# Kernel optimization log

Hardware: AMD Instinct MI355X
Metric: run time of the kernel (lower is better)

The kernel has to match this reference:

```python
import jax, jax.numpy as jnp
import numpy as np

N_PARENTS = 8
CHILDREN_PER_PARENT = 7
N_CHILDREN = N_PARENTS * CHILDREN_PER_PARENT  # 56 leaf classes
TOTAL_NODES = N_PARENTS + N_CHILDREN          # 64
BATCH = 262144


def _build_state_space():
    """Faithful port of generate_state_space for levels==2.

    Row 0 is the all-zero root state; then for each parent, one parent-only
    row, followed by one (parent, child) row per child. Shape [65, 64].
    """
    S = np.zeros((TOTAL_NODES + 1, TOTAL_NODES), dtype=np.float32)
    recorded = np.zeros(TOTAL_NODES)
    ii = 1
    for c in range(N_CHILDREN):
        p = N_CHILDREN + c // CHILDREN_PER_PARENT  # parent ids 56..63
        if recorded[p] == 0:
            S[ii, p] = 1.0
            recorded[p] = 1
            ii += 1
        S[ii, p] = 1.0
        S[ii, c] = 1.0
        ii += 1
    assert ii == TOTAL_NODES + 1, 'Invalid State Space'
    return jnp.asarray(S)


def setup_inputs() -> dict:
    key = jax.random.key(0)
    k1, k2 = jax.random.split(key)
    pred_label = jax.random.normal(k1, (BATCH, TOTAL_NODES), dtype=jnp.float32)
    gt_label = jax.random.randint(k2, (BATCH,), 0, N_CHILDREN, dtype=jnp.int32)
    return {
        'pred_label': pred_label,
        'gt_label': gt_label,
        'state_space': _build_state_space(),
    }


def reference(pred_label, gt_label, state_space):
    # index[s, b] = <state_space row s, pred_label[b]>  -> [S+1, B]
    index = state_space @ pred_label.T
    joint = jnp.exp(index)                      # [S+1, B]
    z = jnp.sum(joint, axis=0)                  # [B] partition function
    # Vectorized replacement of the per-sample Python loop:
    # rows of the state space that contain the ground-truth node.
    mask = state_space[:, gt_label] > 0         # [S+1, B]
    marginal = jnp.sum(jnp.where(mask, joint, jnp.zeros((), joint.dtype)), axis=0)  # [B]
    loss = -jnp.log(marginal / z)               # [B]
    return jnp.mean(loss)
```

## Files before the change

### kernel.cpp

```cpp
#include <hip/hip_runtime.h>


#define RPB     256
#define THREADS 256

__device__ __forceinline__ float elem(const float4& v, int j) {
    return j == 0 ? v.x : j == 1 ? v.y : j == 2 ? v.z : v.w;
}

__global__ void __launch_bounds__(THREADS) tree_loss_partial(
    const float* __restrict__ pred,
    const int*   __restrict__ gt,
    float*       __restrict__ partial,
    int rows)
{
    __shared__ float wsum[THREADS / 64];

    const int t   = threadIdx.x;
    const int row = blockIdx.x * RPB + t;

    float loss = 0.0f;
    if (row < rows) {
        const float4* p4 = (const float4*)(pred + (size_t)row * 64);

        float4 v[16];
        #pragma unroll
        for (int i = 0; i < 16; ++i) v[i] = p4[i];

        float S[8];
        #pragma unroll
        for (int p = 0; p < 8; ++p) S[p] = 0.0f;
        #pragma unroll
        for (int i = 0; i < 14; ++i) {
            #pragma unroll
            for (int j = 0; j < 4; ++j) {
                constexpr int dummy = 0; (void)dummy;
                const int col = 4 * i + j;
                S[col / 7] += __expf(elem(v[i], j));
            }
        }
        float z = 1.0f;
        #pragma unroll
        for (int p = 0; p < 8; ++p) {
            const int i = (56 + p) >> 2, j = (56 + p) & 3;
            z += __expf(elem(v[i], j)) * (1.0f + S[p]);
        }

        int g = gt[row];
        float xg = pred[(size_t)row * 64 + g];
        float xp = pred[(size_t)row * 64 + 56 + g / 7];
        loss = __logf(z) - xg - xp;
    }

    #pragma unroll
    for (int off = 32; off; off >>= 1) loss += __shfl_xor(loss, off);
    if ((t & 63) == 0) wsum[t >> 6] = loss;
    __syncthreads();
    if (t == 0) {
        float b = 0.0f;
        #pragma unroll
        for (int w = 0; w < THREADS / 64; ++w) b += wsum[w];
        partial[blockIdx.x] = b;
    }
}

__global__ void __launch_bounds__(256) tree_loss_final(
    const float* __restrict__ partial, int n,
    float* __restrict__ out, float inv)
{
    float s = 0.0f;
    for (int i = threadIdx.x; i < n; i += 256) s += partial[i];
    #pragma unroll
    for (int off = 32; off; off >>= 1) s += __shfl_xor(s, off);
    __shared__ float w[4];
    const int lane = threadIdx.x & 63;
    const int wv   = threadIdx.x >> 6;
    if (lane == 0) w[wv] = s;
    __syncthreads();
    if (threadIdx.x == 0) out[0] = (w[0] + w[1] + w[2] + w[3]) * inv;
}

extern "C" void kernel_launch(void* const* d_in, const int* in_sizes, int n_in,
                              void* d_out, int out_size, void* d_ws, size_t ws_size,
                              hipStream_t stream) {
    const float* pred = (const float*)d_in[0];
    const int*   gt   = (const int*)d_in[1];
    float* out     = (float*)d_out;
    float* partial = (float*)d_ws;
    const int rows = in_sizes[1];

    const int blocks = (rows + RPB - 1) / RPB;
    tree_loss_partial<<<blocks, THREADS, 0, stream>>>(pred, gt, partial, rows);
    tree_loss_final<<<1, 256, 0, stream>>>(partial, blocks, out, 1.0f / (float)rows);
}
```

Before: 24.56 us.

## Coalesce row loads via wave-cooperative LDS staging with two lanes per row

Each wave now cooperatively loads 32 contiguous rows with fully coalesced float4 loads, writes exp values into padded shared memory, and then has two lanes per row compute half of the partition sum each, combined with a shuffle. This replaces per-thread strided 256-byte row reads, which coalesce poorly, plus the separate scattered gathers of the ground-truth logits. The cost is LDS traffic, a doubled block count with half the rows per block, and the log of the marginal now being computed from exponentials, which can lose precision.

```diff
diff --git a/kernel.cpp b/kernel.cpp
--- a/kernel.cpp
+++ b/kernel.cpp
@@ -1,12 +1,10 @@
 #include <hip/hip_runtime.h>
 
 
-#define RPB     256
 #define THREADS 256
-
-__device__ __forceinline__ float elem(const float4& v, int j) {
-    return j == 0 ? v.x : j == 1 ? v.y : j == 2 ? v.z : v.w;
-}
+#define WROWS   32
+#define RPB     (4 * WROWS)
+#define STRIDE  65
 
 __global__ void __launch_bounds__(THREADS) tree_loss_partial(
     const float* __restrict__ pred,
@@ -14,54 +12,62 @@
     float*       __restrict__ partial,
     int rows)
 {
-    __shared__ float wsum[THREADS / 64];
+    __shared__ float lds[4 * WROWS * STRIDE];
+    __shared__ float wsum[4];
 
-    const int t   = threadIdx.x;
-    const int row = blockIdx.x * RPB + t;
+    const int t = threadIdx.x;
+    const int w = t >> 6;
+    const int l = t & 63;
+    const int waveRowBase = blockIdx.x * RPB + w * WROWS;
+    float* e_base = &lds[w * WROWS * STRIDE];
 
-    float loss = 0.0f;
-    if (row < rows) {
-        const float4* p4 = (const float4*)(pred + (size_t)row * 64);
+    const float4* p4 = (const float4*)pred + (size_t)waveRowBase * 16;
+    const bool full = (waveRowBase + WROWS <= rows);
+    float4 v[8];
+    #pragma unroll
+    for (int i = 0; i < 8; ++i) {
+        const int f = i * 64 + l;
+        v[i] = (full || waveRowBase + (f >> 4) < rows)
+                 ? p4[f] : make_float4(0.f, 0.f, 0.f, 0.f);
+    }
+    #pragma unroll
+    for (int i = 0; i < 8; ++i) {
+        const int f   = i * 64 + l;
+        const int row = f >> 4;
+        const int c4  = (f & 15) << 2;
+        float* dst = e_base + row * STRIDE + c4;
+        dst[0] = __expf(v[i].x); dst[1] = __expf(v[i].y);
+        dst[2] = __expf(v[i].z); dst[3] = __expf(v[i].w);
+    }
 
-        float4 v[16];
+    const int r  = l & 31;
+    const int hi = l >> 5;
+    const float* e  = e_base + r * STRIDE;
+    const float* ec = e + hi * 28;
+    const float* ep = e + 56 + hi * 4;
+    float zh = 0.f;
+    #pragma unroll
+    for (int p = 0; p < 4; ++p) {
+        float s = 1.f;
         #pragma unroll
-        for (int i = 0; i < 16; ++i) v[i] = p4[i];
+        for (int c = 0; c < 7; ++c) s += ec[p * 7 + c];
+        zh += ep[p] * s;
+    }
+    const float zo = __shfl_xor(zh, 32);
 
-        float S[8];
-        #pragma unroll
-        for (int p = 0; p < 8; ++p) S[p] = 0.0f;
-        #pragma unroll
-        for (int i = 0; i < 14; ++i) {
-            #pragma unroll
-            for (int j = 0; j < 4; ++j) {
-                constexpr int dummy = 0; (void)dummy;
-                const int col = 4 * i + j;
-                S[col / 7] += __expf(elem(v[i], j));
-            }
-        }
-        float z = 1.0f;
-        #pragma unroll
-        for (int p = 0; p < 8; ++p) {
-            const int i = (56 + p) >> 2, j = (56 + p) & 3;
-            z += __expf(elem(v[i], j)) * (1.0f + S[p]);
-        }
-
-        int g = gt[row];
-        float xg = pred[(size_t)row * 64 + g];
-        float xp = pred[(size_t)row * 64 + 56 + g / 7];
-        loss = __logf(z) - xg - xp;
-    }
+    const int rowg = waveRowBase + r;
+    const bool valid = (rowg < rows);
+    const int g = valid ? gt[rowg] : 0;
+    const float z = 1.f + zh + zo;
+    const float m = e[g] * e[56 + g / 7];
+    float loss = __logf(z / m);
+    loss = (hi == 0 && valid) ? loss : 0.f;
 
     #pragma unroll
     for (int off = 32; off; off >>= 1) loss += __shfl_xor(loss, off);
-    if ((t & 63) == 0) wsum[t >> 6] = loss;
+    if (l == 0) wsum[w] = loss;
     __syncthreads();
-    if (t == 0) {
-        float b = 0.0f;
-        #pragma unroll
-        for (int w = 0; w < THREADS / 64; ++w) b += wsum[w];
-        partial[blockIdx.x] = b;
-    }
+    if (t == 0) partial[blockIdx.x] = wsum[0] + wsum[1] + wsum[2] + wsum[3];
 }
 
 __global__ void __launch_bounds__(256) tree_loss_final(
```

After: 21.65 us. 1.13x faster.
